# Performance work log

Hardware: AMD Instinct MI355X
Metric: run time of the kernel (lower is better)

Reference implementation:

```python
import jax, jax.numpy as jnp
import numpy as np

D_MODEL = 1024
NUM_HEADS = 16
D_K = D_MODEL // NUM_HEADS


def setup_inputs() -> dict:
    key = jax.random.key(0)
    ks = jax.random.split(key, 9)
    B, S = 4, 2048
    scale = 1.0 / np.sqrt(D_MODEL)
    x = jax.random.normal(ks[0], (B, S, D_MODEL), dtype=jnp.float32)
    Wq = jax.random.normal(ks[1], (D_MODEL, D_MODEL), dtype=jnp.float32) * scale
    Wk = jax.random.normal(ks[2], (D_MODEL, D_MODEL), dtype=jnp.float32) * scale
    Wv = jax.random.normal(ks[3], (D_MODEL, D_MODEL), dtype=jnp.float32) * scale
    Wo = jax.random.normal(ks[4], (D_MODEL, D_MODEL), dtype=jnp.float32) * scale
    bq = jax.random.normal(ks[5], (D_MODEL,), dtype=jnp.float32) * 0.01
    bk = jax.random.normal(ks[6], (D_MODEL,), dtype=jnp.float32) * 0.01
    bv = jax.random.normal(ks[7], (D_MODEL,), dtype=jnp.float32) * 0.01
    bo = jax.random.normal(ks[8], (D_MODEL,), dtype=jnp.float32) * 0.01
    return {"x": x, "Wq": Wq, "bq": bq, "Wk": Wk, "bk": bk,
            "Wv": Wv, "bv": bv, "Wo": Wo, "bo": bo}


def reference(x, Wq, bq, Wk, bk, Wv, bv, Wo, bo):
    B, S, _ = x.shape
    # Linear projections (torch Linear: y = x @ W.T + b; here W stored as [in,out])
    q = (x @ Wq + bq).reshape(B, S, NUM_HEADS, D_K).transpose(0, 2, 1, 3)  # [B,H,S,dk]
    k = (x @ Wk + bk).reshape(B, S, NUM_HEADS, D_K).transpose(0, 2, 1, 3)
    v = (x @ Wv + bv).reshape(B, S, NUM_HEADS, D_K).transpose(0, 2, 1, 3)
    scores = jnp.einsum('bhqd,bhkd->bhqk', q, k) / jnp.sqrt(jnp.float32(D_K))
    causal = jnp.triu(jnp.ones((S, S), dtype=bool), k=1)  # True above diagonal
    scores = jnp.where(causal, -jnp.inf, scores)
    attn = jax.nn.softmax(scores, axis=-1)
    out = jnp.einsum('bhqk,bhkd->bhqd', attn, v)  # dropout is identity in eval
    out = out.transpose(0, 2, 1, 3).reshape(B, S, D_MODEL)
    return out @ Wo + bo
```

## Files before the change

### kernel.cpp

```cpp
#include <hip/hip_runtime.h>

typedef __bf16 bf16;
typedef __bf16 bf16x8 __attribute__((ext_vector_type(8)));
typedef float f32x4 __attribute__((ext_vector_type(4)));

#define DM 1024
#define NH 16
#define DKK 64
#define BB 4
#define SS 2048
#define MTOT (BB * SS)
#define QSC 0.18033688011112042f

__device__ __forceinline__ f32x4 mfma16(bf16x8 a, bf16x8 b, f32x4 c) {
  return __builtin_amdgcn_mfma_f32_16x16x32_bf16(a, b, c, 0, 0, 0);
}

__device__ __forceinline__ int pswz(int row, int colbyte) {
  return row * 128 + (colbyte ^ ((row & 7) << 4));
}

__global__ void cvt_kernel(const float* __restrict__ in, bf16* __restrict__ out) {
  long i = (long)(blockIdx.x * blockDim.x + threadIdx.x) * 8;
  float4 a = *reinterpret_cast<const float4*>(in + i);
  float4 b = *reinterpret_cast<const float4*>(in + i + 4);
  bf16x8 o;
  o[0] = (bf16)a.x; o[1] = (bf16)a.y; o[2] = (bf16)a.z; o[3] = (bf16)a.w;
  o[4] = (bf16)b.x; o[5] = (bf16)b.y; o[6] = (bf16)b.z; o[7] = (bf16)b.w;
  *reinterpret_cast<bf16x8*>(out + i) = o;
}

__global__ void transpose_cvt_kernel(const float* __restrict__ w0, const float* __restrict__ w1,
                                     const float* __restrict__ w2, const float* __restrict__ w3,
                                     bf16* __restrict__ o0, bf16* __restrict__ o1,
                                     bf16* __restrict__ o2, bf16* __restrict__ o3) {
  __shared__ float t[32][33];
  int z = blockIdx.z;
  const float* src = z == 0 ? w0 : z == 1 ? w1 : z == 2 ? w2 : w3;
  bf16* dst = z == 0 ? o0 : z == 1 ? o1 : z == 2 ? o2 : o3;
  int n0 = blockIdx.x * 32, k0 = blockIdx.y * 32;
  int tx = threadIdx.x, ty = threadIdx.y;
#pragma unroll
  for (int j = 0; j < 4; ++j)
    t[ty + 8 * j][tx] = src[(long)(k0 + ty + 8 * j) * DM + n0 + tx];
  __syncthreads();
#pragma unroll
  for (int j = 0; j < 4; ++j)
    dst[(long)(n0 + ty + 8 * j) * DM + k0 + tx] = (bf16)t[tx][ty + 8 * j];
}

template <int MODE>
__global__ __launch_bounds__(256, 2) void gemm_kernel(const bf16* __restrict__ A,
                                                      const bf16* __restrict__ Bt,
                                                      const float* __restrict__ bias,
                                                      void* __restrict__ Cout, float oscale) {
  const int LDT = 40;
  __shared__ bf16 As[2][128 * LDT];
  __shared__ bf16 Bs[2][128 * LDT];
  int tid = threadIdx.x;
  int m0 = blockIdx.x * 128, n0 = blockIdx.y * 128;
  int lane = tid & 63, wid = tid >> 6;
  int wr = wid >> 1, wc = wid & 1;
  int lo = lane & 15, hi = lane >> 4;
  int r0 = tid >> 2, c0 = (tid & 3) * 8;
  const bf16* Ap = A + (long)(m0 + r0) * DM + c0;
  const bf16* Bp = Bt + (long)(n0 + r0) * DM + c0;
  int lA = r0 * LDT + c0;
  int lA2 = (r0 + 64) * LDT + c0;

  f32x4 acc[4][4] = {};

  int4 ra0 = *(const int4*)Ap;
  int4 ra1 = *(const int4*)(Ap + 64 * DM);
  int4 rb0 = *(const int4*)Bp;
  int4 rb1 = *(const int4*)(Bp + 64 * DM);
  *(int4*)&As[0][lA] = ra0; *(int4*)&As[0][lA2] = ra1;
  *(int4*)&Bs[0][lA] = rb0; *(int4*)&Bs[0][lA2] = rb1;
  __syncthreads();

  int buf = 0;
  for (int kt = 0; kt < 32; ++kt) {
    int4 na0, na1, nb0, nb1;
    bool more = (kt + 1) < 32;
    if (more) {
      const bf16* Ap2 = Ap + (kt + 1) * 32;
      const bf16* Bp2 = Bp + (kt + 1) * 32;
      na0 = *(const int4*)Ap2; na1 = *(const int4*)(Ap2 + 64 * DM);
      nb0 = *(const int4*)Bp2; nb1 = *(const int4*)(Bp2 + 64 * DM);
    }
    bf16x8 af[4], bfr[4];
#pragma unroll
    for (int mi = 0; mi < 4; ++mi)
      af[mi] = *(const bf16x8*)&As[buf][(wr * 64 + mi * 16 + lo) * LDT + hi * 8];
#pragma unroll
    for (int ni = 0; ni < 4; ++ni)
      bfr[ni] = *(const bf16x8*)&Bs[buf][(wc * 64 + ni * 16 + lo) * LDT + hi * 8];
#pragma unroll
    for (int mi = 0; mi < 4; ++mi)
#pragma unroll
      for (int ni = 0; ni < 4; ++ni)
        acc[mi][ni] = mfma16(af[mi], bfr[ni], acc[mi][ni]);
    if (more) {
      *(int4*)&As[buf ^ 1][lA] = na0; *(int4*)&As[buf ^ 1][lA2] = na1;
      *(int4*)&Bs[buf ^ 1][lA] = nb0; *(int4*)&Bs[buf ^ 1][lA2] = nb1;
    }
    __syncthreads();
    buf ^= 1;
  }

#pragma unroll
  for (int ni = 0; ni < 4; ++ni) {
    int col = n0 + wc * 64 + ni * 16 + lo;
    float bv = bias[col];
#pragma unroll
    for (int mi = 0; mi < 4; ++mi) {
      int rowb = m0 + wr * 64 + mi * 16 + hi * 4;
#pragma unroll
      for (int r = 0; r < 4; ++r) {
        int row = rowb + r;
        float v = (acc[mi][ni][r] + bv) * oscale;
        if (MODE == 0) {
          int b = row >> 11, s = row & 2047, h = col >> 6, d = col & 63;
          ((bf16*)Cout)[(((long)(b * NH + h) * SS + s) << 6) | d] = (bf16)v;
        } else if (MODE == 1) {
          int b = row >> 11, s = row & 2047, h = col >> 6, d = col & 63;
          ((bf16*)Cout)[(((long)(b * NH + h) * DKK + d) << 11) | s] = (bf16)v;
        } else {
          ((float*)Cout)[(long)row * DM + col] = v;
        }
      }
    }
  }
}

__global__ __launch_bounds__(256, 2) void attn_kernel(const bf16* __restrict__ Q,
                                                      const bf16* __restrict__ K,
                                                      const bf16* __restrict__ VT,
                                                      bf16* __restrict__ AO) {
  __shared__ char Pl[4][4096];
  int bid = blockIdx.x;
  int qt = 15 - (bid >> 6);
  int bh = bid & 63;
  int tid = threadIdx.x, wid = tid >> 6, lane = tid & 63;
  int lo = lane & 15, hi = lane >> 4;
  int q0w = qt * 128 + wid * 32;
  const bf16* Qh = Q + (long)bh * SS * DKK;
  const bf16* Kh = K + (long)bh * SS * DKK;
  const bf16* Vh = VT + (long)bh * DKK * SS;
  char* pw = Pl[wid];

  bf16x8 qf[2][2];
#pragma unroll
  for (int b2 = 0; b2 < 2; ++b2)
#pragma unroll
    for (int c = 0; c < 2; ++c)
      qf[b2][c] = *(const bf16x8*)&Qh[(q0w + b2 * 16 + lo) * DKK + c * 32 + hi * 8];

  f32x4 o[4][2] = {};
  float mrun[2][4], lrun[2][4];
#pragma unroll
  for (int b2 = 0; b2 < 2; ++b2)
#pragma unroll
    for (int r = 0; r < 4; ++r) { mrun[b2][r] = -1e30f; lrun[b2][r] = 0.f; }

  int ntiles = (q0w + 95) >> 6;
  for (int t = 0; t < ntiles; ++t) {
    int kb = t * 64;
    f32x4 s[2][4];
#pragma unroll
    for (int kf = 0; kf < 4; ++kf) {
      const bf16* kp = &Kh[(kb + kf * 16 + lo) * DKK + hi * 8];
      bf16x8 k0 = *(const bf16x8*)kp;
      bf16x8 k1 = *(const bf16x8*)(kp + 32);
#pragma unroll
      for (int b2 = 0; b2 < 2; ++b2) {
        f32x4 z = {0.f, 0.f, 0.f, 0.f};
        s[b2][kf] = mfma16(qf[b2][1], k1, mfma16(qf[b2][0], k0, z));
      }
    }

    if (t == ntiles - 1) {
#pragma unroll
      for (int b2 = 0; b2 < 2; ++b2)
#pragma unroll
        for (int kf = 0; kf < 4; ++kf) {
          int kcol = kb + kf * 16 + lo;
#pragma unroll
          for (int r = 0; r < 4; ++r) {
            int qrow = q0w + b2 * 16 + hi * 4 + r;
            if (kcol > qrow) s[b2][kf][r] = -1e30f;
          }
        }
    }

    float pm[2][4];
#pragma unroll
    for (int b2 = 0; b2 < 2; ++b2)
#pragma unroll
      for (int r = 0; r < 4; ++r)
        pm[b2][r] = fmaxf(fmaxf(s[b2][0][r], s[b2][1][r]),
                          fmaxf(s[b2][2][r], s[b2][3][r]));
#pragma unroll
    for (int m = 1; m < 16; m <<= 1)
#pragma unroll
      for (int b2 = 0; b2 < 2; ++b2)
#pragma unroll
        for (int r = 0; r < 4; ++r)
          pm[b2][r] = fmaxf(pm[b2][r], __shfl_xor(pm[b2][r], m, 64));

    float rs[2][4];
#pragma unroll
    for (int b2 = 0; b2 < 2; ++b2)
#pragma unroll
      for (int r = 0; r < 4; ++r) {
        float mnew = fmaxf(mrun[b2][r], pm[b2][r]);
        float corr = exp2f(mrun[b2][r] - mnew);
        mrun[b2][r] = mnew;
        lrun[b2][r] *= corr;
#pragma unroll
        for (int df = 0; df < 4; ++df) o[df][b2][r] *= corr;
        int row = b2 * 16 + hi * 4 + r;
        float rsv = 0.f;
#pragma unroll
        for (int kf = 0; kf < 4; ++kf) {
          float p = exp2f(s[b2][kf][r] - mnew);
          rsv += p;
          *(bf16*)(pw + pswz(row, (kf * 16 + lo) * 2)) = (bf16)p;
        }
        rs[b2][r] = rsv;
      }
#pragma unroll
    for (int m = 1; m < 16; m <<= 1)
#pragma unroll
      for (int b2 = 0; b2 < 2; ++b2)
#pragma unroll
        for (int r = 0; r < 4; ++r)
          rs[b2][r] += __shfl_xor(rs[b2][r], m, 64);
#pragma unroll
    for (int b2 = 0; b2 < 2; ++b2)
#pragma unroll
      for (int r = 0; r < 4; ++r) lrun[b2][r] += rs[b2][r];

#pragma unroll
    for (int kk = 0; kk < 2; ++kk) {
      bf16x8 pf[2];
#pragma unroll
      for (int b2 = 0; b2 < 2; ++b2)
        pf[b2] = *(const bf16x8*)(pw + pswz(b2 * 16 + lo, kk * 64 + hi * 16));
#pragma unroll
      for (int df = 0; df < 4; ++df) {
        bf16x8 vf = *(const bf16x8*)&Vh[(df * 16 + lo) * SS + kb + kk * 32 + hi * 8];
#pragma unroll
        for (int b2 = 0; b2 < 2; ++b2)
          o[df][b2] = mfma16(pf[b2], vf, o[df][b2]);
      }
    }
  }

  int b = bh >> 4, h = bh & 15;
#pragma unroll
  for (int b2 = 0; b2 < 2; ++b2)
#pragma unroll
    for (int df = 0; df < 4; ++df)
#pragma unroll
      for (int r = 0; r < 4; ++r) {
        int q = q0w + b2 * 16 + hi * 4 + r;
        AO[(((long)(b * SS + q)) << 10) + h * DKK + df * 16 + lo] =
            (bf16)(o[df][b2][r] / lrun[b2][r]);
      }
}

extern "C" void kernel_launch(void* const* d_in, const int* in_sizes, int n_in,
                              void* d_out, int out_size, void* d_ws, size_t ws_size,
                              hipStream_t stream) {
  if (ws_size < (72ULL << 20)) return;

  const float* x  = (const float*)d_in[0];
  const float* Wq = (const float*)d_in[1];
  const float* bq = (const float*)d_in[2];
  const float* Wk = (const float*)d_in[3];
  const float* bk = (const float*)d_in[4];
  const float* Wv = (const float*)d_in[5];
  const float* bv = (const float*)d_in[6];
  const float* Wo = (const float*)d_in[7];
  const float* bo = (const float*)d_in[8];

  char* ws = (char*)d_ws;
  bf16* xb  = (bf16*)(ws);
  bf16* wtq = (bf16*)(ws + (16L << 20));
  bf16* wtk = (bf16*)(ws + (18L << 20));
  bf16* wtv = (bf16*)(ws + (20L << 20));
  bf16* wto = (bf16*)(ws + (22L << 20));
  bf16* Qb  = (bf16*)(ws + (24L << 20));
  bf16* Kb  = (bf16*)(ws + (40L << 20));
  bf16* VTb = (bf16*)(ws + (56L << 20));
  bf16* AO  = xb;

  cvt_kernel<<<(MTOT * DM) / (256 * 8), 256, 0, stream>>>(x, xb);
  transpose_cvt_kernel<<<dim3(32, 32, 4), dim3(32, 8), 0, stream>>>(
      Wq, Wk, Wv, Wo, wtq, wtk, wtv, wto);

  gemm_kernel<0><<<dim3(64, 8), 256, 0, stream>>>(xb, wtq, bq, (void*)Qb, QSC);
  gemm_kernel<0><<<dim3(64, 8), 256, 0, stream>>>(xb, wtk, bk, (void*)Kb, 1.0f);
  gemm_kernel<1><<<dim3(64, 8), 256, 0, stream>>>(xb, wtv, bv, (void*)VTb, 1.0f);

  attn_kernel<<<dim3(1024), 256, 0, stream>>>(Qb, Kb, VTb, AO);

  gemm_kernel<2><<<dim3(64, 8), 256, 0, stream>>>(AO, wto, bo, d_out, 1.0f);
}
```

Measured before the change: 417.5 us.

## Load GEMM tiles directly into LDS and raise attention occupancy

The projection GEMM now stages its A and B tiles with global_load_lds, which writes global data straight into LDS. This replaces the register round-trip and the separate LDS stores, and it drops the padded row stride so the layout matches the per-wave DMA pattern. Without that padding, the ds_read fragment loads may hit LDS bank conflicts. The attention kernel's launch bounds go from 2 to 4 blocks per CU, which caps its registers per thread and risks spills. Its final normalisation now computes one reciprocal per row and multiplies, instead of dividing per element.

```diff
diff --git a/kernel.cpp b/kernel.cpp
--- a/kernel.cpp
+++ b/kernel.cpp
@@ -14,6 +14,11 @@
 
 __device__ __forceinline__ f32x4 mfma16(bf16x8 a, bf16x8 b, f32x4 c) {
   return __builtin_amdgcn_mfma_f32_16x16x32_bf16(a, b, c, 0, 0, 0);
+}
+
+__device__ __forceinline__ void gload_lds(const bf16* g, void* l) {
+  __builtin_amdgcn_global_load_lds((const __attribute__((address_space(1))) void*)g,
+                                   (__attribute__((address_space(3))) void*)l, 16, 0, 0);
 }
 
 __device__ __forceinline__ int pswz(int row, int colbyte) {
@@ -54,56 +59,51 @@
                                                       const bf16* __restrict__ Bt,
                                                       const float* __restrict__ bias,
                                                       void* __restrict__ Cout, float oscale) {
-  const int LDT = 40;
-  __shared__ bf16 As[2][128 * LDT];
-  __shared__ bf16 Bs[2][128 * LDT];
+  __shared__ bf16 As[2][128 * 32];
+  __shared__ bf16 Bs[2][128 * 32];
   int tid = threadIdx.x;
   int m0 = blockIdx.x * 128, n0 = blockIdx.y * 128;
   int lane = tid & 63, wid = tid >> 6;
   int wr = wid >> 1, wc = wid & 1;
   int lo = lane & 15, hi = lane >> 4;
-  int r0 = tid >> 2, c0 = (tid & 3) * 8;
-  const bf16* Ap = A + (long)(m0 + r0) * DM + c0;
-  const bf16* Bp = Bt + (long)(n0 + r0) * DM + c0;
-  int lA = r0 * LDT + c0;
-  int lA2 = (r0 + 64) * LDT + c0;
+
+  int srow0 = 32 * wid + (lane >> 2);
+  int scol = (lane & 3) * 8;
+  const bf16* Ap0 = A + (long)(m0 + srow0) * DM + scol;
+  const bf16* Ap1 = A + (long)(m0 + srow0 + 16) * DM + scol;
+  const bf16* Bp0 = Bt + (long)(n0 + srow0) * DM + scol;
+  const bf16* Bp1 = Bt + (long)(n0 + srow0 + 16) * DM + scol;
+  int cb0 = (2 * wid) * 1024, cb1 = (2 * wid + 1) * 1024;
 
   f32x4 acc[4][4] = {};
 
-  int4 ra0 = *(const int4*)Ap;
-  int4 ra1 = *(const int4*)(Ap + 64 * DM);
-  int4 rb0 = *(const int4*)Bp;
-  int4 rb1 = *(const int4*)(Bp + 64 * DM);
-  *(int4*)&As[0][lA] = ra0; *(int4*)&As[0][lA2] = ra1;
-  *(int4*)&Bs[0][lA] = rb0; *(int4*)&Bs[0][lA2] = rb1;
+  gload_lds(Ap0, (char*)As[0] + cb0);
+  gload_lds(Ap1, (char*)As[0] + cb1);
+  gload_lds(Bp0, (char*)Bs[0] + cb0);
+  gload_lds(Bp1, (char*)Bs[0] + cb1);
   __syncthreads();
 
   int buf = 0;
   for (int kt = 0; kt < 32; ++kt) {
-    int4 na0, na1, nb0, nb1;
-    bool more = (kt + 1) < 32;
-    if (more) {
-      const bf16* Ap2 = Ap + (kt + 1) * 32;
-      const bf16* Bp2 = Bp + (kt + 1) * 32;
-      na0 = *(const int4*)Ap2; na1 = *(const int4*)(Ap2 + 64 * DM);
-      nb0 = *(const int4*)Bp2; nb1 = *(const int4*)(Bp2 + 64 * DM);
+    if (kt + 1 < 32) {
+      int off = (kt + 1) * 32;
+      gload_lds(Ap0 + off, (char*)As[buf ^ 1] + cb0);
+      gload_lds(Ap1 + off, (char*)As[buf ^ 1] + cb1);
+      gload_lds(Bp0 + off, (char*)Bs[buf ^ 1] + cb0);
+      gload_lds(Bp1 + off, (char*)Bs[buf ^ 1] + cb1);
     }
     bf16x8 af[4], bfr[4];
 #pragma unroll
     for (int mi = 0; mi < 4; ++mi)
-      af[mi] = *(const bf16x8*)&As[buf][(wr * 64 + mi * 16 + lo) * LDT + hi * 8];
+      af[mi] = *(const bf16x8*)&As[buf][(wr * 64 + mi * 16 + lo) * 32 + hi * 8];
 #pragma unroll
     for (int ni = 0; ni < 4; ++ni)
-      bfr[ni] = *(const bf16x8*)&Bs[buf][(wc * 64 + ni * 16 + lo) * LDT + hi * 8];
+      bfr[ni] = *(const bf16x8*)&Bs[buf][(wc * 64 + ni * 16 + lo) * 32 + hi * 8];
 #pragma unroll
     for (int mi = 0; mi < 4; ++mi)
 #pragma unroll
       for (int ni = 0; ni < 4; ++ni)
         acc[mi][ni] = mfma16(af[mi], bfr[ni], acc[mi][ni]);
-    if (more) {
-      *(int4*)&As[buf ^ 1][lA] = na0; *(int4*)&As[buf ^ 1][lA2] = na1;
-      *(int4*)&Bs[buf ^ 1][lA] = nb0; *(int4*)&Bs[buf ^ 1][lA2] = nb1;
-    }
     __syncthreads();
     buf ^= 1;
   }
@@ -133,7 +133,7 @@
   }
 }
 
-__global__ __launch_bounds__(256, 2) void attn_kernel(const bf16* __restrict__ Q,
+__global__ __launch_bounds__(256, 4) void attn_kernel(const bf16* __restrict__ Q,
                                                       const bf16* __restrict__ K,
                                                       const bf16* __restrict__ VT,
                                                       bf16* __restrict__ AO) {
@@ -258,6 +258,11 @@
   }
 
   int b = bh >> 4, h = bh & 15;
+  float linv[2][4];
+#pragma unroll
+  for (int b2 = 0; b2 < 2; ++b2)
+#pragma unroll
+    for (int r = 0; r < 4; ++r) linv[b2][r] = 1.0f / lrun[b2][r];
 #pragma unroll
   for (int b2 = 0; b2 < 2; ++b2)
 #pragma unroll
@@ -266,7 +271,7 @@
       for (int r = 0; r < 4; ++r) {
         int q = q0w + b2 * 16 + hi * 4 + r;
         AO[(((long)(b * SS + q)) << 10) + h * DKK + df * 16 + lo] =
-            (bf16)(o[df][b2][r] / lrun[b2][r]);
+            (bf16)(o[df][b2][r] * linv[b2][r]);
       }
 }
 
```

Measured after the change: 516.8 us. +23.8%, slower.
